# Performance work log

Hardware: AMD Instinct MI355X
Metric: run time of the kernel (lower is better)

Reference implementation:

```python
import jax, jax.numpy as jnp
import numpy as np

MASK_BIAS = 2.0
TEMPERATURE = 1.0


def setup_inputs() -> dict:
    key = jax.random.key(0)
    k1, k2, k3 = jax.random.split(key, 3)
    B, C, D, H, W = 2, 128, 48, 96, 96
    feat = jax.random.normal(k1, (B, C, D, H, W), dtype=jnp.float32)
    mask = jax.random.uniform(k2, (B, 1, D, H, W), dtype=jnp.float32)
    w_attn = jax.random.normal(k3, (C,), dtype=jnp.float32) * (1.0 / np.sqrt(C))
    return {"feat": feat, "mask": mask, "w_attn": w_attn}


def reference(feat, mask, w_attn):
    B, C = feat.shape[:2]
    # 1x1x1 conv with 1 output channel, no bias == channel dot product
    logits = jnp.einsum('bcdhw,c->bdhw', feat, w_attn)  # [B, D, H, W]
    logits = logits + MASK_BIAS * jnp.clip(mask[:, 0], 0.0, 1.0)
    w = jax.nn.softmax((logits / TEMPERATURE).reshape(B, -1), axis=-1)  # [B, N]
    feat_flat = feat.reshape(B, C, -1)  # [B, C, N]
    return jnp.einsum('bcn,bn->bc', feat_flat, w)
```

## Files before the change

kernel.cpp:

```cpp
#include <hip/hip_runtime.h>

constexpr int C   = 128;
constexpr int N   = 48 * 96 * 96;
constexpr int B   = 2;
constexpr int NPB = 256;
constexpr int BPB = N / NPB;
constexpr int REC = 132;

template <int CTRL, int RM>
__device__ __forceinline__ float dpp_add_step(float x) {
    int y = __builtin_amdgcn_update_dpp(0, __float_as_int(x), CTRL, RM, 0xF, true);
    return x + __int_as_float(y);
}

__device__ __forceinline__ float wave_sum64(float x) {
    x = dpp_add_step<0xB1, 0xF>(x);
    x = dpp_add_step<0x4E, 0xF>(x);
    x = dpp_add_step<0x141, 0xF>(x);
    x = dpp_add_step<0x140, 0xF>(x);
    x = dpp_add_step<0x142, 0xA>(x);
    x = dpp_add_step<0x143, 0xC>(x);
    return x;
}

__global__ __launch_bounds__(256, 3) void attn_pool_pass1(
    const float* __restrict__ feat, const float* __restrict__ mask,
    const float* __restrict__ w, float* __restrict__ rec)
{
    const int tid = threadIdx.x;
    const int blk = blockIdx.x;
    const int b   = blk / BPB;
    const int n   = (blk % BPB) * NPB + tid;

    const float* fp = feat + (size_t)b * C * N + n;

    float f[C];
    float logit = 0.f;
#pragma unroll
    for (int c = 0; c < C; ++c) {
        f[c] = fp[(size_t)c * N];
        logit = fmaf(f[c], w[c], logit);
    }
    float mv = mask[(size_t)b * N + n];
    mv = fminf(fmaxf(mv, 0.f), 1.f);
    logit += 2.0f * mv;

    const int lane = tid & 63;
    const int wv   = tid >> 6;
    __shared__ float rmax[4];
    __shared__ float rsum[4];
    __shared__ float SRed[4][C];

    float m = logit;
#pragma unroll
    for (int off = 32; off; off >>= 1) m = fmaxf(m, __shfl_xor(m, off, 64));
    if (lane == 0) rmax[wv] = m;
    __syncthreads();
    m = fmaxf(fmaxf(rmax[0], rmax[1]), fmaxf(rmax[2], rmax[3]));

    const float p = __expf(logit - m);
    float l = p;
#pragma unroll
    for (int off = 32; off; off >>= 1) l += __shfl_xor(l, off, 64);
    if (lane == 0) rsum[wv] = l;

    const bool lastlane = (lane == 63);
#pragma unroll
    for (int c = 0; c < C; ++c) {
        float v = wave_sum64(f[c] * p);
        if (lastlane) SRed[wv][c] = v;
    }
    __syncthreads();

    float* out = rec + (size_t)blk * REC;
    if (tid < C) {
        out[4 + tid] = SRed[0][tid] + SRed[1][tid] + SRed[2][tid] + SRed[3][tid];
    } else if (tid == C) {
        out[0] = m;
        out[1] = rsum[0] + rsum[1] + rsum[2] + rsum[3];
    }
}

__global__ __launch_bounds__(256) void attn_pool_pass2(
    const float* __restrict__ rec, float* __restrict__ out)
{
    const int b    = blockIdx.x;
    const int tid  = threadIdx.x;
    const int lane = tid & 63;
    const int wv   = tid >> 6;
    const float* base = rec + (size_t)b * BPB * REC;

    __shared__ float sc[BPB];
    __shared__ float r4[4];
    __shared__ float racc[C];

    float m = -3.4e38f;
    for (int i = tid; i < BPB; i += 256) m = fmaxf(m, base[(size_t)i * REC]);
#pragma unroll
    for (int off = 32; off; off >>= 1) m = fmaxf(m, __shfl_xor(m, off, 64));
    if (lane == 0) r4[wv] = m;
    __syncthreads();
    const float M = fmaxf(fmaxf(r4[0], r4[1]), fmaxf(r4[2], r4[3]));
    __syncthreads();

    float z = 0.f;
    for (int i = tid; i < BPB; i += 256) {
        float e = __expf(base[(size_t)i * REC] - M);
        sc[i] = e;
        z = fmaf(base[(size_t)i * REC + 1], e, z);
    }
#pragma unroll
    for (int off = 32; off; off >>= 1) z += __shfl_xor(z, off, 64);
    if (lane == 0) r4[wv] = z;
    __syncthreads();
    const float Z = r4[0] + r4[1] + r4[2] + r4[3];

    const int c    = tid & (C - 1);
    const int half = tid >> 7;
    float acc = 0.f;
    const int i0 = half * (BPB / 2), i1 = i0 + (BPB / 2);
    for (int i = i0; i < i1; ++i)
        acc = fmaf(base[(size_t)i * REC + 4 + c], sc[i], acc);
    if (half == 1) racc[c] = acc;
    __syncthreads();
    if (half == 0) out[b * C + c] = (acc + racc[c]) / Z;
}

extern "C" void kernel_launch(void* const* d_in, const int* in_sizes, int n_in,
                              void* d_out, int out_size, void* d_ws, size_t ws_size,
                              hipStream_t stream)
{
    const float* feat = (const float*)d_in[0];
    const float* mask = (const float*)d_in[1];
    const float* w    = (const float*)d_in[2];
    float* rec = (float*)d_ws;

    attn_pool_pass1<<<B * BPB, 256, 0, stream>>>(feat, mask, w, rec);
    attn_pool_pass2<<<B, 256, 0, stream>>>(rec, (float*)d_out);
}
```

Before: 653.2 us.

## Split channels across waves with float4 positions to cut registers and reductions

Pass 1 now gives each of 8 waves a 16-channel slice while each lane holds 4 contiguous positions, loaded as float4. Partial logits are combined through shared memory, and each wave runs only 16 cross-lane reductions instead of 128. This lowers register pressure, raises occupancy and widens memory transactions, at the cost of an extra LDS exchange and barrier. Pass 2 is widened to 1024 threads and reads separate max/sum and channel-sum arrays.

```diff
diff --git a/kernel.cpp b/kernel.cpp
--- a/kernel.cpp
+++ b/kernel.cpp
@@ -3,16 +3,16 @@
 constexpr int C   = 128;
 constexpr int N   = 48 * 96 * 96;
 constexpr int B   = 2;
-constexpr int NPB = 256;
-constexpr int BPB = N / NPB;
-constexpr int REC = 132;
+constexpr int P   = 256;
+constexpr int BPB = N / P;
+constexpr int G   = 16;
+constexpr int NW  = 8;
 
 template <int CTRL, int RM>
 __device__ __forceinline__ float dpp_add_step(float x) {
     int y = __builtin_amdgcn_update_dpp(0, __float_as_int(x), CTRL, RM, 0xF, true);
     return x + __int_as_float(y);
 }
-
 __device__ __forceinline__ float wave_sum64(float x) {
     x = dpp_add_step<0xB1, 0xF>(x);
     x = dpp_add_step<0x4E, 0xF>(x);
@@ -23,107 +23,144 @@
     return x;
 }
 
-__global__ __launch_bounds__(256, 3) void attn_pool_pass1(
+__global__ __launch_bounds__(512, 4) void attn_pool_pass1(
     const float* __restrict__ feat, const float* __restrict__ mask,
-    const float* __restrict__ w, float* __restrict__ rec)
+    const float* __restrict__ w, float* __restrict__ Sout, float* __restrict__ ml)
 {
     const int tid = threadIdx.x;
+    const int wv  = tid >> 6;
+    const int t   = tid & 63;
     const int blk = blockIdx.x;
     const int b   = blk / BPB;
-    const int n   = (blk % BPB) * NPB + tid;
+    const int n0  = (blk % BPB) * P;
+    const int cb  = wv * G;
 
-    const float* fp = feat + (size_t)b * C * N + n;
+    const float* fbase = feat + (size_t)b * C * N + n0 + 4 * t;
 
-    float f[C];
-    float logit = 0.f;
+    __shared__ float4 plog[NW][64];
+    __shared__ float  rmax[NW];
+    __shared__ float  rsum1;
+    __shared__ float  SRed[NW][G];
+
+    float4 f[G];
+    float4 pl = make_float4(0.f, 0.f, 0.f, 0.f);
 #pragma unroll
-    for (int c = 0; c < C; ++c) {
-        f[c] = fp[(size_t)c * N];
-        logit = fmaf(f[c], w[c], logit);
+    for (int c = 0; c < G; ++c) {
+        f[c] = *reinterpret_cast<const float4*>(fbase + (size_t)(cb + c) * N);
+        const float wc = w[cb + c];
+        pl.x = fmaf(f[c].x, wc, pl.x);
+        pl.y = fmaf(f[c].y, wc, pl.y);
+        pl.z = fmaf(f[c].z, wc, pl.z);
+        pl.w = fmaf(f[c].w, wc, pl.w);
     }
-    float mv = mask[(size_t)b * N + n];
-    mv = fminf(fmaxf(mv, 0.f), 1.f);
-    logit += 2.0f * mv;
+    if (wv == 0) {
+        float4 mv = *reinterpret_cast<const float4*>(mask + (size_t)b * N + n0 + 4 * t);
+        pl.x += 2.f * fminf(fmaxf(mv.x, 0.f), 1.f);
+        pl.y += 2.f * fminf(fmaxf(mv.y, 0.f), 1.f);
+        pl.z += 2.f * fminf(fmaxf(mv.z, 0.f), 1.f);
+        pl.w += 2.f * fminf(fmaxf(mv.w, 0.f), 1.f);
+    }
+    plog[wv][t] = pl;
+    __syncthreads();
 
-    const int lane = tid & 63;
-    const int wv   = tid >> 6;
-    __shared__ float rmax[4];
-    __shared__ float rsum[4];
-    __shared__ float SRed[4][C];
+    float4 lg = plog[0][t];
+#pragma unroll
+    for (int g = 1; g < NW; ++g) {
+        float4 q = plog[g][t];
+        lg.x += q.x; lg.y += q.y; lg.z += q.z; lg.w += q.w;
+    }
 
-    float m = logit;
+    float m = fmaxf(fmaxf(lg.x, lg.y), fmaxf(lg.z, lg.w));
 #pragma unroll
     for (int off = 32; off; off >>= 1) m = fmaxf(m, __shfl_xor(m, off, 64));
-    if (lane == 0) rmax[wv] = m;
+    if (t == 0) rmax[wv] = m;
     __syncthreads();
-    m = fmaxf(fmaxf(rmax[0], rmax[1]), fmaxf(rmax[2], rmax[3]));
+    m = fmaxf(fmaxf(fmaxf(rmax[0], rmax[1]), fmaxf(rmax[2], rmax[3])),
+              fmaxf(fmaxf(rmax[4], rmax[5]), fmaxf(rmax[6], rmax[7])));
 
-    const float p = __expf(logit - m);
-    float l = p;
+    const float p0 = __expf(lg.x - m), p1 = __expf(lg.y - m);
+    const float p2 = __expf(lg.z - m), p3 = __expf(lg.w - m);
+
+    if (wv == 0) {
+        float l = ((p0 + p1) + (p2 + p3));
 #pragma unroll
-    for (int off = 32; off; off >>= 1) l += __shfl_xor(l, off, 64);
-    if (lane == 0) rsum[wv] = l;
+        for (int off = 32; off; off >>= 1) l += __shfl_xor(l, off, 64);
+        if (t == 0) rsum1 = l;
+    }
 
-    const bool lastlane = (lane == 63);
 #pragma unroll
-    for (int c = 0; c < C; ++c) {
-        float v = wave_sum64(f[c] * p);
-        if (lastlane) SRed[wv][c] = v;
+    for (int c = 0; c < G; ++c) {
+        float s = f[c].x * p0;
+        s = fmaf(f[c].y, p1, s);
+        s = fmaf(f[c].z, p2, s);
+        s = fmaf(f[c].w, p3, s);
+        s = wave_sum64(s);
+        if (t == 63) SRed[wv][c] = s;
     }
     __syncthreads();
 
-    float* out = rec + (size_t)blk * REC;
     if (tid < C) {
-        out[4 + tid] = SRed[0][tid] + SRed[1][tid] + SRed[2][tid] + SRed[3][tid];
+        Sout[(size_t)blk * C + tid] = SRed[tid >> 4][tid & 15];
     } else if (tid == C) {
-        out[0] = m;
-        out[1] = rsum[0] + rsum[1] + rsum[2] + rsum[3];
+        ml[2 * blk]     = m;
+        ml[2 * blk + 1] = rsum1;
     }
 }
 
-__global__ __launch_bounds__(256) void attn_pool_pass2(
-    const float* __restrict__ rec, float* __restrict__ out)
+__global__ __launch_bounds__(1024) void attn_pool_pass2(
+    const float* __restrict__ S, const float* __restrict__ ml,
+    float* __restrict__ out)
 {
     const int b    = blockIdx.x;
     const int tid  = threadIdx.x;
     const int lane = tid & 63;
     const int wv   = tid >> 6;
-    const float* base = rec + (size_t)b * BPB * REC;
+    const float* mlb = ml + (size_t)b * BPB * 2;
+    const float* Sb  = S  + (size_t)b * BPB * C;
 
     __shared__ float sc[BPB];
-    __shared__ float r4[4];
-    __shared__ float racc[C];
+    __shared__ float redA[16], redB[16];
+    __shared__ float racc[8][C];
 
     float m = -3.4e38f;
-    for (int i = tid; i < BPB; i += 256) m = fmaxf(m, base[(size_t)i * REC]);
+    for (int i = tid; i < BPB; i += 1024) m = fmaxf(m, mlb[2 * i]);
 #pragma unroll
     for (int off = 32; off; off >>= 1) m = fmaxf(m, __shfl_xor(m, off, 64));
-    if (lane == 0) r4[wv] = m;
+    if (lane == 0) redA[wv] = m;
     __syncthreads();
-    const float M = fmaxf(fmaxf(r4[0], r4[1]), fmaxf(r4[2], r4[3]));
-    __syncthreads();
+    float M = redA[0];
+#pragma unroll
+    for (int k = 1; k < 16; ++k) M = fmaxf(M, redA[k]);
 
     float z = 0.f;
-    for (int i = tid; i < BPB; i += 256) {
-        float e = __expf(base[(size_t)i * REC] - M);
+    for (int i = tid; i < BPB; i += 1024) {
+        float e = __expf(mlb[2 * i] - M);
         sc[i] = e;
-        z = fmaf(base[(size_t)i * REC + 1], e, z);
+        z = fmaf(mlb[2 * i + 1], e, z);
     }
 #pragma unroll
     for (int off = 32; off; off >>= 1) z += __shfl_xor(z, off, 64);
-    if (lane == 0) r4[wv] = z;
+    if (lane == 0) redB[wv] = z;
     __syncthreads();
-    const float Z = r4[0] + r4[1] + r4[2] + r4[3];
+    float Z = redB[0];
+#pragma unroll
+    for (int k = 1; k < 16; ++k) Z += redB[k];
 
-    const int c    = tid & (C - 1);
-    const int half = tid >> 7;
+    const int c  = tid & (C - 1);
+    const int ck = tid >> 7;
+    const int i0 = ck * (BPB / 8), i1 = i0 + (BPB / 8);
     float acc = 0.f;
-    const int i0 = half * (BPB / 2), i1 = i0 + (BPB / 2);
     for (int i = i0; i < i1; ++i)
-        acc = fmaf(base[(size_t)i * REC + 4 + c], sc[i], acc);
-    if (half == 1) racc[c] = acc;
+        acc = fmaf(Sb[(size_t)i * C + c], sc[i], acc);
+    racc[ck][c] = acc;
     __syncthreads();
-    if (half == 0) out[b * C + c] = (acc + racc[c]) / Z;
+
+    if (tid < C) {
+        float tot = 0.f;
+#pragma unroll
+        for (int k = 0; k < 8; ++k) tot += racc[k][tid];
+        out[b * C + tid] = tot / Z;
+    }
 }
 
 extern "C" void kernel_launch(void* const* d_in, const int* in_sizes, int n_in,
@@ -133,8 +170,10 @@
     const float* feat = (const float*)d_in[0];
     const float* mask = (const float*)d_in[1];
     const float* w    = (const float*)d_in[2];
-    float* rec = (float*)d_ws;
 
-    attn_pool_pass1<<<B * BPB, 256, 0, stream>>>(feat, mask, w, rec);
-    attn_pool_pass2<<<B, 256, 0, stream>>>(rec, (float*)d_out);
+    float* Sout = (float*)d_ws;
+    float* ml   = Sout + (size_t)B * BPB * C;
+
+    attn_pool_pass1<<<B * BPB, 512, 0, stream>>>(feat, mask, w, Sout, ml);
+    attn_pool_pass2<<<B, 1024, 0, stream>>>(Sout, ml, (float*)d_out);
 }
```

Measured after the change: 589.6 us. 9.7% less time.
